# Kernel optimization log

Measured on AMD Instinct MI355X. Metric: run time of the kernel, lower is better.

Reference implementation:

```python
import jax, jax.numpy as jnp
from jax import lax
import numpy as np

B, T, F = 128, 512, 256
H = 1024
GHOST = 512  # hidden_size - hidden_size // ghost_ratio
INTR = 512   # hidden_size // ghost_ratio


def setup_inputs() -> dict:
    key = jax.random.key(0)
    ks = jax.random.split(key, 8)
    stdv = 1.0 / np.sqrt(H)
    u = lambda k, shape: jax.random.uniform(k, shape, jnp.float32, -stdv, stdv)
    return {
        "x": jax.random.normal(ks[0], (B, T, F), jnp.float32),
        "hidden": jax.random.normal(ks[1], (B, 1, H), jnp.float32),
        "weight_gate": u(ks[2], (2 * INTR, F + H)),
        "weight_candidate": u(ks[3], (INTR, F + H)),
        "weight_ghost": u(ks[4], (GHOST, INTR)),
        "bias_gate": u(ks[5], (2 * INTR,)),
        "bias_candidate": u(ks[6], (INTR,)),
        "bias_ghost": jax.random.normal(ks[7], (GHOST,), jnp.float32),
    }


def reference(x, hidden, weight_gate, weight_candidate, weight_ghost,
              bias_gate, bias_candidate, bias_ghost):
    ghost_size = weight_ghost.shape[0]
    h0 = hidden[:, 0, :]  # squeeze(1) -> [B, H]

    def step(h, x_t):
        # gates: [B, F+H] @ [F+H, 2*INTR]
        gate = jax.nn.sigmoid(
            jnp.concatenate([x_t, h], axis=1) @ weight_gate.T + bias_gate)
        r, u = jnp.split(gate, 2, axis=1)
        r_state = r * h[:, ghost_size:]
        cand_in = jnp.concatenate([x_t, h[:, :ghost_size], r_state], axis=1)
        c = jnp.tanh(cand_in @ weight_candidate.T + bias_candidate)
        new_h = u * h[:, ghost_size:] + (1.0 - u) * c          # [B, INTR]
        ghost = jnp.tanh(new_h @ weight_ghost.T + bias_ghost)  # [B, GHOST]
        nh = jnp.concatenate([ghost, new_h], axis=1)           # [B, H]
        return nh, nh

    xs = jnp.swapaxes(x, 0, 1)  # [T, B, F]
    h_final, outs = lax.scan(step, h0, xs)
    outputs = jnp.swapaxes(outs, 0, 1)  # [B, T, H]
    return outputs, h_final[:, None, :]
```

## Files before the change

kernel.cpp:

```cpp
#include <hip/hip_runtime.h>


typedef unsigned short ushort_t;
typedef unsigned long long ull_t;
typedef __attribute__((ext_vector_type(8))) short short8;
typedef __attribute__((ext_vector_type(4))) float f32x4;

#define NB 128
#define NT 512
#define NF 256
#define NH 1024
#define KGATE 1280

#define AT_LOAD(p)     __hip_atomic_load((p), __ATOMIC_RELAXED, __HIP_MEMORY_SCOPE_AGENT)
#define AT_STORE(p,v)  __hip_atomic_store((p), (v), __ATOMIC_RELAXED, __HIP_MEMORY_SCOPE_AGENT)

__device__ __forceinline__ float bf2f(ushort_t u) {
  union { unsigned int i; float f; } v; v.i = ((unsigned int)u) << 16; return v.f;
}
__device__ __forceinline__ ushort_t f2bf(float f) {
  union { float f; unsigned int i; } v; v.f = f;
  unsigned int r = v.i + 0x7FFFu + ((v.i >> 16) & 1u);
  return (ushort_t)(r >> 16);
}
__device__ __forceinline__ float sigmoidf_(float x) { return 1.f / (1.f + __expf(-x)); }
__device__ __forceinline__ float tanhf_(float x) {
  float e = __expf(2.f * x); return 1.f - 2.f / (e + 1.f);
}

__device__ __forceinline__ void group_barrier(unsigned* cnt, unsigned* go,
                                              unsigned target) {
  __syncthreads();
  if (threadIdx.x == 0) {
    unsigned old = __hip_atomic_fetch_add(cnt, 1u, __ATOMIC_RELAXED,
                                          __HIP_MEMORY_SCOPE_AGENT);
    if (old + 1u == target) {
      AT_STORE(go, target);
    } else {
      while (AT_LOAD(go) < target) { }
    }
  }
  __syncthreads();
}

__device__ __forceinline__ short8 pack_bf16_8(const float* p) {
  float4 a = *(const float4*)p;
  float4 b = *(const float4*)(p + 4);
  short8 f;
  f[0] = (short)f2bf(a.x); f[1] = (short)f2bf(a.y);
  f[2] = (short)f2bf(a.z); f[3] = (short)f2bf(a.w);
  f[4] = (short)f2bf(b.x); f[5] = (short)f2bf(b.y);
  f[6] = (short)f2bf(b.z); f[7] = (short)f2bf(b.w);
  return f;
}

__global__ void __launch_bounds__(256, 1) ghost_gru_persistent(
    const float* __restrict__ x, const float* __restrict__ hidden,
    const float* __restrict__ Wg, const float* __restrict__ Wc,
    const float* __restrict__ Wgh, const float* __restrict__ bg,
    const float* __restrict__ bc, const float* __restrict__ bgh,
    float* __restrict__ out, unsigned int* __restrict__ hbuf_u,
    unsigned int* __restrict__ rs_u, float* __restrict__ ubuf,
    unsigned int* __restrict__ counters)
{
  const int wgid = blockIdx.x;
  const int g    = wgid & 7;
  const int memb = wgid >> 3;
  const int b0   = g * 16;
  const int tid  = threadIdx.x;
  const int wv   = tid >> 6;
  const int lane = tid & 63;
  const int lq   = lane >> 4;
  const int ln   = lane & 15;
  unsigned* cnt = counters + g * 32;
  unsigned* go  = counters + 256 + g * 32;

  __shared__ __align__(16) ushort_t Abuf[16][1800];

  short8 wfrag[40];
  int ncol0;
  float biasv;
  if (wv == 0 || wv == 1) {
    ncol0 = memb * 32 + wv * 16;
    const float* wp = Wg + (size_t)(ncol0 + ln) * KGATE + lq * 8;
    #pragma unroll
    for (int kc = 0; kc < 40; ++kc) wfrag[kc] = pack_bf16_8(wp + kc * 32);
    biasv = bg[ncol0 + ln];
  } else if (wv == 2) {
    ncol0 = memb * 16;
    const float* wp = Wc + (size_t)(ncol0 + ln) * KGATE + lq * 8;
    #pragma unroll
    for (int kc = 0; kc < 40; ++kc) wfrag[kc] = pack_bf16_8(wp + kc * 32);
    biasv = bc[ncol0 + ln];
  } else {
    ncol0 = memb * 16;
    const float* wp = Wgh + (size_t)(ncol0 + ln) * 512 + lq * 8;
    #pragma unroll
    for (int kc = 0; kc < 16; ++kc) wfrag[kc] = pack_bf16_8(wp + kc * 32);
    biasv = bgh[ncol0 + ln];
  }

  float hreg[4];
  if (wv == 2) {
    #pragma unroll
    for (int r = 0; r < 4; ++r)
      hreg[r] = hidden[(size_t)(b0 + lq * 4 + r) * NH + 512 + ncol0 + ln];
  }

  const ull_t* hbuf64 = (const ull_t*)hbuf_u;
  const ull_t* rs64   = (const ull_t*)rs_u;

  {
    ull_t nv[8];
    #pragma unroll
    for (int k = 0; k < 8; ++k) {
      int j = tid + k * 256;
      nv[k] = AT_LOAD(&hbuf64[(size_t)(b0 + (j >> 7)) * 256 + 128 + (j & 127)]);
    }
    #pragma unroll
    for (int k = 0; k < 8; ++k) {
      int j = tid + k * 256;
      *(ull_t*)&Abuf[j >> 7][768 + 4 * (j & 127)] = nv[k];
    }
  }

  float4 xv[4];
  #pragma unroll
  for (int k = 0; k < 4; ++k) {
    int i = tid + k * 256;
    xv[k] = *(const float4*)&x[((size_t)(b0 + (i >> 6)) * NT + 0) * NF + (i & 63) * 4];
  }

  #pragma unroll 1
  for (int t = 0; t < NT; ++t) {
    const int cur = t & 1, nxt = cur ^ 1;
    const ull_t* hsrc64 = hbuf64 + (size_t)cur * NB * 256;
    unsigned*    hdst   = hbuf_u + (size_t)nxt * NB * 512;
    const ull_t* hdst64 = hbuf64 + (size_t)nxt * NB * 256;

    {
      ull_t gv[8];
      #pragma unroll
      for (int k = 0; k < 8; ++k) {
        int j = tid + k * 256;
        gv[k] = AT_LOAD(&hsrc64[(size_t)(b0 + (j >> 7)) * 256 + (j & 127)]);
      }
      #pragma unroll
      for (int k = 0; k < 4; ++k) {
        int i = tid + k * 256;
        int row = i >> 6, c4 = (i & 63) * 4;
        ushort4 u4 = make_ushort4(f2bf(xv[k].x), f2bf(xv[k].y),
                                  f2bf(xv[k].z), f2bf(xv[k].w));
        *(ushort4*)&Abuf[row][c4] = u4;
      }
      #pragma unroll
      for (int k = 0; k < 8; ++k) {
        int j = tid + k * 256;
        *(ull_t*)&Abuf[j >> 7][256 + 4 * (j & 127)] = gv[k];
      }
    }
    __syncthreads();

    {
      const int tn = (t + 1 < NT) ? t + 1 : t;
      #pragma unroll
      for (int k = 0; k < 4; ++k) {
        int i = tid + k * 256;
        xv[k] = *(const float4*)&x[((size_t)(b0 + (i >> 6)) * NT + tn) * NF + (i & 63) * 4];
      }
    }

    if (wv < 2) {
      f32x4 acc0 = {0.f, 0.f, 0.f, 0.f}, acc1 = {0.f, 0.f, 0.f, 0.f};
      #pragma unroll
      for (int kc = 0; kc < 40; kc += 2) {
        short8 a0 = *(const short8*)&Abuf[ln][kc * 32 + lq * 8];
        acc0 = __builtin_amdgcn_mfma_f32_16x16x32_bf16(a0, wfrag[kc], acc0, 0, 0, 0);
        short8 a1 = *(const short8*)&Abuf[ln][(kc + 1) * 32 + lq * 8];
        acc1 = __builtin_amdgcn_mfma_f32_16x16x32_bf16(a1, wfrag[kc + 1], acc1, 0, 0, 0);
      }
      const int n = ncol0 + ln;
      if (ncol0 < 512) {
        #pragma unroll
        for (int r = 0; r < 4; ++r) {
          int row = lq * 4 + r;
          float s = sigmoidf_(acc0[r] + acc1[r] + biasv);
          float hold = bf2f(Abuf[row][768 + n]);
          unsigned hv = (unsigned)f2bf(s * hold);
          unsigned pv = (unsigned)__shfl_xor((int)hv, 1);
          if (!(ln & 1))
            AT_STORE(&rs_u[(size_t)(b0 + row) * 256 + (n >> 1)], hv | (pv << 16));
        }
      } else {
        #pragma unroll
        for (int r = 0; r < 4; ++r) {
          int row = lq * 4 + r;
          float s = sigmoidf_(acc0[r] + acc1[r] + biasv);
          AT_STORE(&ubuf[(size_t)(b0 + row) * 512 + (n - 512)], s);
        }
      }
    }
    group_barrier(cnt, go, 32u * (3u * (unsigned)t + 1u));

    float uval[4];
    f32x4 acc0c = {0.f, 0.f, 0.f, 0.f}, acc1c = {0.f, 0.f, 0.f, 0.f};
    if (wv == 2) {
      #pragma unroll
      for (int r = 0; r < 4; ++r)
        uval[r] = AT_LOAD(&ubuf[(size_t)(b0 + lq * 4 + r) * 512 + ncol0 + ln]);
      #pragma unroll
      for (int kc = 0; kc < 24; kc += 2) {
        short8 a0 = *(const short8*)&Abuf[ln][kc * 32 + lq * 8];
        acc0c = __builtin_amdgcn_mfma_f32_16x16x32_bf16(a0, wfrag[kc], acc0c, 0, 0, 0);
        short8 a1 = *(const short8*)&Abuf[ln][(kc + 1) * 32 + lq * 8];
        acc1c = __builtin_amdgcn_mfma_f32_16x16x32_bf16(a1, wfrag[kc + 1], acc1c, 0, 0, 0);
      }
    } else if (wv < 2) {
      ull_t rv[16];
      #pragma unroll
      for (int k = 0; k < 16; ++k) {
        int j = tid + k * 128;
        rv[k] = AT_LOAD(&rs64[(size_t)(b0 + (j >> 7)) * 128 + (j & 127)]);
      }
      #pragma unroll
      for (int k = 0; k < 16; ++k) {
        int j = tid + k * 128;
        *(ull_t*)&Abuf[j >> 7][1280 + 4 * (j & 127)] = rv[k];
      }
    }
    __syncthreads();
    if (wv == 2) {
      #pragma unroll
      for (int kc = 24; kc < 40; kc += 2) {
        short8 a0 = *(const short8*)&Abuf[ln][1280 + (kc - 24) * 32 + lq * 8];
        acc0c = __builtin_amdgcn_mfma_f32_16x16x32_bf16(a0, wfrag[kc], acc0c, 0, 0, 0);
        short8 a1 = *(const short8*)&Abuf[ln][1280 + (kc - 23) * 32 + lq * 8];
        acc1c = __builtin_amdgcn_mfma_f32_16x16x32_bf16(a1, wfrag[kc + 1], acc1c, 0, 0, 0);
      }
      const int n = ncol0 + ln;
      #pragma unroll
      for (int r = 0; r < 4; ++r) {
        int row = lq * 4 + r;
        int b = b0 + row;
        float cv = tanhf_(acc0c[r] + acc1c[r] + biasv);
        float u = uval[r];
        float hnew = u * hreg[r] + (1.f - u) * cv;
        hreg[r] = hnew;
        out[((size_t)b * NT + t) * NH + 512 + n] = hnew;
        unsigned hv = (unsigned)f2bf(hnew);
        unsigned pv = (unsigned)__shfl_xor((int)hv, 1);
        if (!(ln & 1))
          AT_STORE(&hdst[(size_t)b * 512 + 256 + (n >> 1)], hv | (pv << 16));
        if (t == NT - 1) out[(size_t)NB * NT * NH + (size_t)b * NH + 512 + n] = hnew;
      }
    }
    group_barrier(cnt, go, 32u * (3u * (unsigned)t + 2u));

    {
      ull_t nv[8];
      #pragma unroll
      for (int k = 0; k < 8; ++k) {
        int j = tid + k * 256;
        nv[k] = AT_LOAD(&hdst64[(size_t)(b0 + (j >> 7)) * 256 + 128 + (j & 127)]);
      }
      #pragma unroll
      for (int k = 0; k < 8; ++k) {
        int j = tid + k * 256;
        *(ull_t*)&Abuf[j >> 7][768 + 4 * (j & 127)] = nv[k];
      }
    }
    __syncthreads();

    if (wv == 3) {
      f32x4 acc = {0.f, 0.f, 0.f, 0.f};
      #pragma unroll
      for (int kc = 0; kc < 16; ++kc) {
        short8 a = *(const short8*)&Abuf[ln][768 + kc * 32 + lq * 8];
        acc = __builtin_amdgcn_mfma_f32_16x16x32_bf16(a, wfrag[kc], acc, 0, 0, 0);
      }
      const int n = ncol0 + ln;
      #pragma unroll
      for (int r = 0; r < 4; ++r) {
        int row = lq * 4 + r;
        int b = b0 + row;
        float gv = tanhf_(acc[r] + biasv);
        out[((size_t)b * NT + t) * NH + n] = gv;
        unsigned hv = (unsigned)f2bf(gv);
        unsigned pv = (unsigned)__shfl_xor((int)hv, 1);
        if (!(ln & 1))
          AT_STORE(&hdst[(size_t)b * 512 + (n >> 1)], hv | (pv << 16));
        if (t == NT - 1) out[(size_t)NB * NT * NH + (size_t)b * NH + n] = gv;
      }
    }
    group_barrier(cnt, go, 32u * (3u * (unsigned)t + 3u));
  }
}

__global__ void init_kernel(const float* __restrict__ hidden,
                            unsigned int* __restrict__ hbuf_u,
                            unsigned int* __restrict__ counters) {
  int i = blockIdx.x * blockDim.x + threadIdx.x;
  if (i < NB * 512) {
    unsigned lo = (unsigned)f2bf(hidden[2 * i]);
    unsigned hi = (unsigned)f2bf(hidden[2 * i + 1]);
    hbuf_u[i] = lo | (hi << 16);
  }
  if (i < 512) counters[i] = 0;
}

extern "C" void kernel_launch(void* const* d_in, const int* in_sizes, int n_in,
                              void* d_out, int out_size, void* d_ws, size_t ws_size,
                              hipStream_t stream) {
  (void)in_sizes; (void)n_in; (void)out_size; (void)ws_size;
  const float* x      = (const float*)d_in[0];
  const float* hidden = (const float*)d_in[1];
  const float* Wg     = (const float*)d_in[2];
  const float* Wc     = (const float*)d_in[3];
  const float* Wgh    = (const float*)d_in[4];
  const float* bg     = (const float*)d_in[5];
  const float* bc     = (const float*)d_in[6];
  const float* bgh    = (const float*)d_in[7];
  float* out = (float*)d_out;

  char* ws = (char*)d_ws;
  unsigned int* hbuf_u   = (unsigned int*)(ws);
  unsigned int* rs_u     = (unsigned int*)(ws + 524288);
  float*        ubuf     = (float*)(ws + 655360);
  unsigned int* counters = (unsigned int*)(ws + 917504);

  init_kernel<<<dim3(256), dim3(256), 0, stream>>>(hidden, hbuf_u, counters);
  ghost_gru_persistent<<<dim3(256), dim3(256), 0, stream>>>(
      x, hidden, Wg, Wc, Wgh, bg, bc, bgh, out, hbuf_u, rs_u, ubuf, counters);
}
```

Baseline: 4.472 ms.

## Replace counter barrier with per-block flags and keep update gate in LDS

```diff
diff --git a/kernel.cpp b/kernel.cpp
--- a/kernel.cpp
+++ b/kernel.cpp
@@ -28,19 +28,19 @@
   float e = __expf(2.f * x); return 1.f - 2.f / (e + 1.f);
 }
 
-__device__ __forceinline__ void group_barrier(unsigned* cnt, unsigned* go,
-                                              unsigned target) {
+__device__ __forceinline__ void post_flag(unsigned* flags, int memb, unsigned val) {
   __syncthreads();
-  if (threadIdx.x == 0) {
-    unsigned old = __hip_atomic_fetch_add(cnt, 1u, __ATOMIC_RELAXED,
-                                          __HIP_MEMORY_SCOPE_AGENT);
-    if (old + 1u == target) {
-      AT_STORE(go, target);
-    } else {
-      while (AT_LOAD(go) < target) { }
-    }
-  }
-  __syncthreads();
+  if (threadIdx.x == 0) AT_STORE(&flags[memb], val);
+}
+
+__device__ __forceinline__ void wait_flags(const unsigned* flags, unsigned tgt) {
+  const int sl = (int)(threadIdx.x & 31u);
+  for (;;) {
+    unsigned f = AT_LOAD(&flags[sl]);
+    if (__all((int)(f >= tgt))) break;
+    __builtin_amdgcn_s_sleep(1);
+  }
+  __builtin_amdgcn_sched_barrier(0);
 }
 
 __device__ __forceinline__ short8 pack_bf16_8(const float* p) {
@@ -60,8 +60,7 @@
     const float* __restrict__ Wgh, const float* __restrict__ bg,
     const float* __restrict__ bc, const float* __restrict__ bgh,
     float* __restrict__ out, unsigned int* __restrict__ hbuf_u,
-    unsigned int* __restrict__ rs_u, float* __restrict__ ubuf,
-    unsigned int* __restrict__ counters)
+    unsigned int* __restrict__ rs_u, unsigned int* __restrict__ counters)
 {
   const int wgid = blockIdx.x;
   const int g    = wgid & 7;
@@ -72,16 +71,21 @@
   const int lane = tid & 63;
   const int lq   = lane >> 4;
   const int ln   = lane & 15;
-  unsigned* cnt = counters + g * 32;
-  unsigned* go  = counters + 256 + g * 32;
-
-  __shared__ __align__(16) ushort_t Abuf[16][1800];
+  unsigned* flags = counters + g * 64;
+
+  __shared__ __align__(16) ushort_t Abuf[16][1832];
 
   short8 wfrag[40];
   int ncol0;
   float biasv;
-  if (wv == 0 || wv == 1) {
-    ncol0 = memb * 32 + wv * 16;
+  if (wv == 0) {
+    ncol0 = memb * 16;
+    const float* wp = Wg + (size_t)(ncol0 + ln) * KGATE + lq * 8;
+    #pragma unroll
+    for (int kc = 0; kc < 40; ++kc) wfrag[kc] = pack_bf16_8(wp + kc * 32);
+    biasv = bg[ncol0 + ln];
+  } else if (wv == 1) {
+    ncol0 = 512 + memb * 16;
     const float* wp = Wg + (size_t)(ncol0 + ln) * KGATE + lq * 8;
     #pragma unroll
     for (int kc = 0; kc < 40; ++kc) wfrag[kc] = pack_bf16_8(wp + kc * 32);
@@ -180,7 +184,7 @@
         acc1 = __builtin_amdgcn_mfma_f32_16x16x32_bf16(a1, wfrag[kc + 1], acc1, 0, 0, 0);
       }
       const int n = ncol0 + ln;
-      if (ncol0 < 512) {
+      if (wv == 0) {
         #pragma unroll
         for (int r = 0; r < 4; ++r) {
           int row = lq * 4 + r;
@@ -196,18 +200,19 @@
         for (int r = 0; r < 4; ++r) {
           int row = lq * 4 + r;
           float s = sigmoidf_(acc0[r] + acc1[r] + biasv);
-          AT_STORE(&ubuf[(size_t)(b0 + row) * 512 + (n - 512)], s);
+          ((float*)&Abuf[row][1792])[ln] = s;
         }
       }
     }
-    group_barrier(cnt, go, 32u * (3u * (unsigned)t + 1u));
+    post_flag(flags, memb, 3u * (unsigned)t + 1u);
+    wait_flags(flags, 3u * (unsigned)t + 1u);
 
     float uval[4];
     f32x4 acc0c = {0.f, 0.f, 0.f, 0.f}, acc1c = {0.f, 0.f, 0.f, 0.f};
     if (wv == 2) {
       #pragma unroll
       for (int r = 0; r < 4; ++r)
-        uval[r] = AT_LOAD(&ubuf[(size_t)(b0 + lq * 4 + r) * 512 + ncol0 + ln]);
+        uval[r] = ((const float*)&Abuf[lq * 4 + r][1792])[ln];
       #pragma unroll
       for (int kc = 0; kc < 24; kc += 2) {
         short8 a0 = *(const short8*)&Abuf[ln][kc * 32 + lq * 8];
@@ -254,7 +259,8 @@
         if (t == NT - 1) out[(size_t)NB * NT * NH + (size_t)b * NH + 512 + n] = hnew;
       }
     }
-    group_barrier(cnt, go, 32u * (3u * (unsigned)t + 2u));
+    post_flag(flags, memb, 3u * (unsigned)t + 2u);
+    wait_flags(flags, 3u * (unsigned)t + 2u);
 
     {
       ull_t nv[8];
@@ -292,7 +298,8 @@
         if (t == NT - 1) out[(size_t)NB * NT * NH + (size_t)b * NH + n] = gv;
       }
     }
-    group_barrier(cnt, go, 32u * (3u * (unsigned)t + 3u));
+    post_flag(flags, memb, 3u * (unsigned)t + 3u);
+    wait_flags(flags, 3u * (unsigned)t + 3u);
   }
 }
 
@@ -325,10 +332,9 @@
   char* ws = (char*)d_ws;
   unsigned int* hbuf_u   = (unsigned int*)(ws);
   unsigned int* rs_u     = (unsigned int*)(ws + 524288);
-  float*        ubuf     = (float*)(ws + 655360);
-  unsigned int* counters = (unsigned int*)(ws + 917504);
+  unsigned int* counters = (unsigned int*)(ws + 655360);
 
   init_kernel<<<dim3(256), dim3(256), 0, stream>>>(hidden, hbuf_u, counters);
   ghost_gru_persistent<<<dim3(256), dim3(256), 0, stream>>>(
-      x, hidden, Wg, Wc, Wgh, bg, bc, bgh, out, hbuf_u, rs_u, ubuf, counters);
-}
+      x, hidden, Wg, Wc, Wgh, bg, bc, bgh, out, hbuf_u, rs_u, counters);
+}
```

New measurement: 4.060 ms. 1.1x faster.
